# Kernel optimization log

Measured on AMD Instinct MI355X. Metric: run time of the kernel, lower is better.

## Reference

```python
import jax, jax.numpy as jnp
import numpy as np

B, H, W, C = 32, 56, 56, 192
WS, SS, NH = 7, 3, 6
HD = C // NH
SCALE = HD ** -0.5
N = WS * WS
NW = (H // WS) * (W // WS)
EPS = 1e-5


def _rel_pos_index():
    coords = np.stack(np.meshgrid(np.arange(WS), np.arange(WS), indexing='ij'))  # (2,WS,WS)
    cf = coords.reshape(2, -1)
    rel = cf[:, :, None] - cf[:, None, :]  # (2,N,N)
    rel = rel.transpose(1, 2, 0)
    rel[:, :, 0] += WS - 1
    rel[:, :, 1] += WS - 1
    rel[:, :, 0] *= 2 * WS - 1
    return rel.sum(-1)  # (N,N) int


def _attn_mask():
    img = np.zeros((H, W))
    cnt = 0
    for hs in (slice(0, -WS), slice(-WS, -SS), slice(-SS, None)):
        for ws in (slice(0, -WS), slice(-WS, -SS), slice(-SS, None)):
            img[hs, ws] = cnt
            cnt += 1
    win = img.reshape(H // WS, WS, W // WS, WS).transpose(0, 2, 1, 3).reshape(NW, N)
    diff = win[:, None, :] - win[:, :, None]
    return np.where(diff != 0, -100.0, 0.0).astype(np.float32)  # (NW,N,N)


REL_IDX = jnp.asarray(_rel_pos_index())
ATTN_MASK = jnp.asarray(_attn_mask())


def _ln(x, g, b):
    mu = x.mean(-1, keepdims=True)
    var = ((x - mu) ** 2).mean(-1, keepdims=True)
    return (x - mu) * jax.lax.rsqrt(var + EPS) * g + b


def setup_inputs() -> dict:
    key = jax.random.key(0)
    ks = jax.random.split(key, 8)
    d = {
        'x': jax.random.normal(ks[0], (B, H * W, C), jnp.float32),
        'norm1_g': jnp.ones((C,), jnp.float32),
        'norm1_b': jnp.zeros((C,), jnp.float32),
        'qkv_w': jax.random.normal(ks[1], (C, 3 * C), jnp.float32) * 0.02,
        'qkv_b': jnp.zeros((3 * C,), jnp.float32),
        'rpb_table': jax.random.normal(ks[2], ((2 * WS - 1) ** 2, NH), jnp.float32) * 0.02,
        'proj_w': jax.random.normal(ks[3], (C, C), jnp.float32) * 0.02,
        'proj_b': jnp.zeros((C,), jnp.float32),
        'norm2_g': jnp.ones((C,), jnp.float32),
        'norm2_b': jnp.zeros((C,), jnp.float32),
        'fc1_w': jax.random.normal(ks[4], (C, 4 * C), jnp.float32) * 0.02,
        'fc1_b': jnp.zeros((4 * C,), jnp.float32),
        'fc2_w': jax.random.normal(ks[5], (4 * C, C), jnp.float32) * 0.02,
        'fc2_b': jnp.zeros((C,), jnp.float32),
    }
    return d


def reference(x, norm1_g, norm1_b, qkv_w, qkv_b, rpb_table, proj_w, proj_b,
              norm2_g, norm2_b, fc1_w, fc1_b, fc2_w, fc2_b):
    shortcut = x
    h = _ln(x, norm1_g, norm1_b).reshape(B, H, W, C)
    # cyclic shift
    h = jnp.roll(h, (-SS, -SS), axis=(1, 2))
    # window partition -> (B*NW, N, C)
    hw = h.reshape(B, H // WS, WS, W // WS, WS, C).transpose(0, 1, 3, 2, 4, 5)
    hw = hw.reshape(B * NW, N, C)
    # qkv
    qkv = (hw @ qkv_w + qkv_b).reshape(B * NW, N, 3, NH, HD).transpose(2, 0, 3, 1, 4)
    q, k, v = qkv[0], qkv[1], qkv[2]  # (B_, NH, N, HD)
    attn = jnp.einsum('whnd,whmd->whnm', q * SCALE, k)
    bias = rpb_table[REL_IDX.reshape(-1)].reshape(N, N, NH).transpose(2, 0, 1)
    attn = attn + bias[None]
    # shift mask
    attn = attn.reshape(B, NW, NH, N, N) + ATTN_MASK[None, :, None]
    attn = jax.nn.softmax(attn.reshape(B * NW, NH, N, N), axis=-1)
    out = jnp.einsum('whnm,whmd->whnd', attn, v).transpose(0, 2, 1, 3).reshape(B * NW, N, C)
    out = out @ proj_w + proj_b
    # window reverse + unshift
    out = out.reshape(B, H // WS, W // WS, WS, WS, C).transpose(0, 1, 3, 2, 4, 5).reshape(B, H, W, C)
    out = jnp.roll(out, (SS, SS), axis=(1, 2)).reshape(B, H * W, C)
    x = shortcut + out
    # MLP
    m = _ln(x, norm2_g, norm2_b)
    m = jax.nn.gelu(m @ fc1_w + fc1_b, approximate=False) @ fc2_w + fc2_b
    return x + m
```

## Files before the change

### kernel.cpp

```cpp
#include <hip/hip_runtime.h>
#include <hip/hip_bf16.h>
#include <math.h>

#define MTOK 100352
#define SCALE_ 0.17677669529663687f

typedef short bf16x8 __attribute__((ext_vector_type(8)));
typedef float f32x4 __attribute__((ext_vector_type(4)));

__device__ __forceinline__ float b2f(unsigned short u) {
    return __uint_as_float(((unsigned int)u) << 16);
}
__device__ __forceinline__ unsigned short f2b(float f) {
    unsigned int u = __float_as_uint(f);
    unsigned int r = (u + 0x7FFFu + ((u >> 16) & 1u)) >> 16;
    return (unsigned short)r;
}
__device__ __forceinline__ void gload_lds16(const unsigned short* g, unsigned short* l) {
    __builtin_amdgcn_global_load_lds(
        (const __attribute__((address_space(1))) void*)g,
        (__attribute__((address_space(3))) void*)l, 16, 0, 0);
}

__global__ __launch_bounds__(256) void wconv_k(
    const float* __restrict__ w, unsigned short* __restrict__ wt, int K, int N)
{
    const int i = blockIdx.x * 256 + threadIdx.x;
    if (i >= N * K) return;
    const int n = i / K, k = i - n * K;
    wt[i] = f2b(w[(size_t)k * N + n]);
}

__global__ __launch_bounds__(256) void ln1_window_k(
    const float* __restrict__ x, const float* __restrict__ g,
    const float* __restrict__ bt, unsigned short* __restrict__ out)
{
    const int wid = (blockIdx.x * 256 + threadIdx.x) >> 6;
    if (wid >= MTOK) return;
    const int lane = threadIdx.x & 63;
    const int widx = wid / 49, n = wid - widx * 49;
    const int b = widx >> 6, win = widx & 63;
    const int wh = win >> 3, ww = win & 7;
    const int r = n / 7, cc = n - r * 7;
    int hh = wh * 7 + r + 3;  if (hh >= 56) hh -= 56;
    int wc = ww * 7 + cc + 3; if (wc >= 56) wc -= 56;
    const size_t src = ((size_t)b * 3136 + hh * 56 + wc) * 192;
    const float v0 = x[src + lane], v1 = x[src + lane + 64], v2 = x[src + lane + 128];
    float s1 = v0 + v1 + v2;
    float s2 = v0 * v0 + v1 * v1 + v2 * v2;
    #pragma unroll
    for (int off = 32; off; off >>= 1) {
        s1 += __shfl_xor(s1, off, 64);
        s2 += __shfl_xor(s2, off, 64);
    }
    const float mu = s1 * (1.f / 192.f);
    const float var = s2 * (1.f / 192.f) - mu * mu;
    const float rs = rsqrtf(var + 1e-5f);
    const size_t dst = (size_t)wid * 192;
    out[dst + lane]       = f2b((v0 - mu) * rs * g[lane]       + bt[lane]);
    out[dst + lane + 64]  = f2b((v1 - mu) * rs * g[lane + 64]  + bt[lane + 64]);
    out[dst + lane + 128] = f2b((v2 - mu) * rs * g[lane + 128] + bt[lane + 128]);
}

__global__ __launch_bounds__(256) void ln2_k(
    const float* __restrict__ x, const float* __restrict__ g,
    const float* __restrict__ bt, unsigned short* __restrict__ out)
{
    const int t = (blockIdx.x * 256 + threadIdx.x) >> 6;
    if (t >= MTOK) return;
    const int lane = threadIdx.x & 63;
    const size_t src = (size_t)t * 192;
    const float v0 = x[src + lane], v1 = x[src + lane + 64], v2 = x[src + lane + 128];
    float s1 = v0 + v1 + v2;
    float s2 = v0 * v0 + v1 * v1 + v2 * v2;
    #pragma unroll
    for (int off = 32; off; off >>= 1) {
        s1 += __shfl_xor(s1, off, 64);
        s2 += __shfl_xor(s2, off, 64);
    }
    const float mu = s1 * (1.f / 192.f);
    const float var = s2 * (1.f / 192.f) - mu * mu;
    const float rs = rsqrtf(var + 1e-5f);
    out[src + lane]       = f2b((v0 - mu) * rs * g[lane]       + bt[lane]);
    out[src + lane + 64]  = f2b((v1 - mu) * rs * g[lane + 64]  + bt[lane + 64]);
    out[src + lane + 128] = f2b((v2 - mu) * rs * g[lane + 128] + bt[lane + 128]);
}

enum { EPI_STORE_BF16 = 0, EPI_PROJ = 1, EPI_GELU = 2, EPI_RES = 3 };

template <int EPI>
__global__ __launch_bounds__(256) void mgemm_k(
    const unsigned short* __restrict__ A, const unsigned short* __restrict__ BT,
    const float* __restrict__ bias, unsigned short* __restrict__ outb,
    float* __restrict__ outf, const float* __restrict__ xres,
    int N, int K, int gx)
{
    __shared__ __align__(16) unsigned short As[2][128 * 32];
    __shared__ __align__(16) unsigned short Bs[2][64 * 32];

    const int nwg = gridDim.x;
    int lin = blockIdx.x;
    lin = (lin & 7) * (nwg >> 3) + (lin >> 3);
    const int bn = lin % gx, bm = lin / gx;
    const int row0 = bm * 128, col0 = bn * 64;

    const int tid = threadIdx.x;
    const int w = tid >> 6, lane = tid & 63;
    const int wr = w >> 1, wc = w & 1;
    const int l16 = lane & 15, l4 = lane >> 4;

    const unsigned short* Ab = A + (size_t)row0 * K;
    const unsigned short* Bb = BT + (size_t)col0 * K;
    const int sr = lane >> 2;
    const int sq = ((lane & 3) ^ ((lane >> 3) & 3)) * 8;

    #pragma unroll
    for (int i = 0; i < 2; i++) {
        const int ch = w * 2 + i;
        gload_lds16(Ab + (size_t)(ch * 16 + sr) * K + sq, &As[0][ch * 512 + lane * 8]);
    }
    gload_lds16(Bb + (size_t)(w * 16 + sr) * K + sq, &Bs[0][w * 512 + lane * 8]);
    __syncthreads();

    f32x4 acc[4][2];
    #pragma unroll
    for (int m = 0; m < 4; m++)
        #pragma unroll
        for (int n = 0; n < 2; n++) acc[m][n] = (f32x4){0.f, 0.f, 0.f, 0.f};

    const int rdc = (l4 ^ ((l16 >> 1) & 3)) * 8;
    const int nt = K >> 5;
    for (int t = 0; t < nt; ++t) {
        const int cur = t & 1;
        if (t + 1 < nt) {
            const int k0 = (t + 1) << 5;
            #pragma unroll
            for (int i = 0; i < 2; i++) {
                const int ch = w * 2 + i;
                gload_lds16(Ab + (size_t)(ch * 16 + sr) * K + k0 + sq,
                            &As[cur ^ 1][ch * 512 + lane * 8]);
            }
            gload_lds16(Bb + (size_t)(w * 16 + sr) * K + k0 + sq,
                        &Bs[cur ^ 1][w * 512 + lane * 8]);
        }
        bf16x8 af[4], bf[2];
        #pragma unroll
        for (int m = 0; m < 4; m++)
            af[m] = *reinterpret_cast<const bf16x8*>(
                &As[cur][(wr * 64 + m * 16 + l16) * 32 + rdc]);
        #pragma unroll
        for (int n = 0; n < 2; n++)
            bf[n] = *reinterpret_cast<const bf16x8*>(
                &Bs[cur][(wc * 32 + n * 16 + l16) * 32 + rdc]);
        #pragma unroll
        for (int m = 0; m < 4; m++)
            #pragma unroll
            for (int n = 0; n < 2; n++)
                acc[m][n] = __builtin_amdgcn_mfma_f32_16x16x32_bf16(
                    af[m], bf[n], acc[m][n], 0, 0, 0);
        __syncthreads();
    }

    float bv[2];
    #pragma unroll
    for (int n = 0; n < 2; n++) bv[n] = bias[col0 + wc * 32 + n * 16 + l16];

    #pragma unroll
    for (int m = 0; m < 4; m++) {
        #pragma unroll
        for (int j = 0; j < 4; j++) {
            const int row = row0 + wr * 64 + m * 16 + l4 * 4 + j;
            if constexpr (EPI == EPI_PROJ) {
                const int widx = row / 49, n49 = row - widx * 49;
                const int b = widx >> 6, win = widx & 63;
                const int wh = win >> 3, ww = win & 7;
                const int r = n49 / 7, cc = n49 - r * 7;
                int hh = wh * 7 + r + 3;  if (hh >= 56) hh -= 56;
                int wcc = ww * 7 + cc + 3; if (wcc >= 56) wcc -= 56;
                const size_t tok = ((size_t)b * 3136 + hh * 56 + wcc) * 192;
                #pragma unroll
                for (int n = 0; n < 2; n++) {
                    const int col = col0 + wc * 32 + n * 16 + l16;
                    outf[tok + col] = xres[tok + col] + acc[m][n][j] + bv[n];
                }
            } else if constexpr (EPI == EPI_STORE_BF16) {
                #pragma unroll
                for (int n = 0; n < 2; n++) {
                    const int col = col0 + wc * 32 + n * 16 + l16;
                    outb[(size_t)row * N + col] = f2b(acc[m][n][j] + bv[n]);
                }
            } else if constexpr (EPI == EPI_GELU) {
                #pragma unroll
                for (int n = 0; n < 2; n++) {
                    const int col = col0 + wc * 32 + n * 16 + l16;
                    float v = acc[m][n][j] + bv[n];
                    v = 0.5f * v * (1.f + erff(v * 0.70710678118654752f));
                    outb[(size_t)row * N + col] = f2b(v);
                }
            } else {
                #pragma unroll
                for (int n = 0; n < 2; n++) {
                    const int col = col0 + wc * 32 + n * 16 + l16;
                    outf[(size_t)row * N + col] += acc[m][n][j] + bv[n];
                }
            }
        }
    }
}

__global__ __launch_bounds__(64) void attn_mfma_k(
    const unsigned short* __restrict__ qkv, const float* __restrict__ rpb,
    unsigned short* __restrict__ out)
{
    const int blk = blockIdx.x;
    const int widx = blk / 6, head = blk - widx * 6;
    const int win = widx & 63;
    const int wh = win >> 3, ww = win & 7;

    __shared__ __align__(16) unsigned short vt[32 * 72];
    __shared__ __align__(16) unsigned short pl[64 * 72];
    __shared__ float bias_s[256];

    const int lane = threadIdx.x;
    const int l16 = lane & 15, l4 = lane >> 4;
    const size_t base = (size_t)widx * 49 * 576 + (size_t)head * 32;

    for (int i = lane; i < 169; i += 64) bias_s[i] = rpb[i * 6 + head];

    #pragma unroll
    for (int it = 0; it < 4; ++it) {
        const int c = lane + it * 64;
        const int m = c >> 2, d8 = (c & 3) * 8;
        bf16x8 v8 = {};
        if (m < 49)
            v8 = *reinterpret_cast<const bf16x8*>(qkv + base + (size_t)m * 576 + 384 + d8);
        #pragma unroll
        for (int r = 0; r < 8; ++r) vt[(d8 + r) * 72 + m] = (unsigned short)v8[r];
    }

    bf16x8 kf[4], qf[4];
    #pragma unroll
    for (int f = 0; f < 4; ++f) {
        const int rrow = f * 16 + l16;
        bf16x8 kz = {}, qz = {};
        if (rrow < 49) {
            kz = *reinterpret_cast<const bf16x8*>(qkv + base + (size_t)rrow * 576 + 192 + l4 * 8);
            qz = *reinterpret_cast<const bf16x8*>(qkv + base + (size_t)rrow * 576 + l4 * 8);
        }
        kf[f] = kz; qf[f] = qz;
    }

    f32x4 acc[4][4];
    #pragma unroll
    for (int mf = 0; mf < 4; ++mf)
        #pragma unroll
        for (int nf = 0; nf < 4; ++nf) {
            f32x4 z = (f32x4){0.f, 0.f, 0.f, 0.f};
            acc[mf][nf] = __builtin_amdgcn_mfma_f32_16x16x32_bf16(kf[mf], qf[nf], z, 0, 0, 0);
        }

    __syncthreads();

    int gn[4], labn[4]; bool nok[4];
    #pragma unroll
    for (int nf = 0; nf < 4; ++nf) {
        const int n = nf * 16 + l16;
        const int rn = (n * 9363) >> 16, cn = n - rn * 7;
        gn[nf] = n + 6 * rn;
        labn[nf] = (wh == 7 ? (rn < 4 ? 1 : 2) : 0) * 3 + (ww == 7 ? (cn < 4 ? 1 : 2) : 0);
        nok[nf] = (n < 49);
    }

    #pragma unroll
    for (int mf = 0; mf < 4; ++mf) {
        #pragma unroll
        for (int j = 0; j < 4; ++j) {
            const int m = mf * 16 + l4 * 4 + j;
            const int rm = (m * 9363) >> 16, cm = m - rm * 7;
            const int gm = m + 6 * rm;
            const int labm = (wh == 7 ? (rm < 4 ? 1 : 2) : 0) * 3 + (ww == 7 ? (cm < 4 ? 1 : 2) : 0);
            const bool mok = (m < 49);
            #pragma unroll
            for (int nf = 0; nf < 4; ++nf) {
                float s = -1e30f;
                if (mok && nok[nf]) {
                    s = acc[mf][nf][j] * SCALE_ + bias_s[gn[nf] - gm + 84];
                    if (labn[nf] != labm) s -= 100.f;
                }
                acc[mf][nf][j] = s;
            }
        }
    }

    #pragma unroll
    for (int nf = 0; nf < 4; ++nf) {
        float mx = -1e30f;
        #pragma unroll
        for (int mf = 0; mf < 4; ++mf)
            #pragma unroll
            for (int j = 0; j < 4; ++j) mx = fmaxf(mx, acc[mf][nf][j]);
        mx = fmaxf(mx, __shfl_xor(mx, 16, 64));
        mx = fmaxf(mx, __shfl_xor(mx, 32, 64));
        float sum = 0.f;
        #pragma unroll
        for (int mf = 0; mf < 4; ++mf)
            #pragma unroll
            for (int j = 0; j < 4; ++j) {
                const float e = __expf(acc[mf][nf][j] - mx);
                acc[mf][nf][j] = e;
                sum += e;
            }
        sum += __shfl_xor(sum, 16, 64);
        sum += __shfl_xor(sum, 32, 64);
        const float inv = 1.f / sum;
        const int n = nf * 16 + l16;
        #pragma unroll
        for (int mf = 0; mf < 4; ++mf)
            #pragma unroll
            for (int jp = 0; jp < 2; ++jp) {
                const int m = mf * 16 + l4 * 4 + jp * 2;
                const unsigned int pk =
                    (unsigned int)f2b(acc[mf][nf][jp * 2] * inv) |
                    ((unsigned int)f2b(acc[mf][nf][jp * 2 + 1] * inv) << 16);
                *reinterpret_cast<unsigned int*>(&pl[n * 72 + m]) = pk;
            }
    }
    __syncthreads();

    f32x4 oacc[4][2];
    #pragma unroll
    for (int nf = 0; nf < 4; ++nf)
        #pragma unroll
        for (int df = 0; df < 2; ++df) oacc[nf][df] = (f32x4){0.f, 0.f, 0.f, 0.f};
    #pragma unroll
    for (int ks = 0; ks < 2; ++ks) {
        bf16x8 vf[2];
        #pragma unroll
        for (int df = 0; df < 2; ++df)
            vf[df] = *reinterpret_cast<const bf16x8*>(&vt[(df * 16 + l16) * 72 + ks * 32 + l4 * 8]);
        #pragma unroll
        for (int nf = 0; nf < 4; ++nf) {
            const bf16x8 pf = *reinterpret_cast<const bf16x8*>(&pl[(nf * 16 + l16) * 72 + ks * 32 + l4 * 8]);
            #pragma unroll
            for (int df = 0; df < 2; ++df)
                oacc[nf][df] = __builtin_amdgcn_mfma_f32_16x16x32_bf16(pf, vf[df], oacc[nf][df], 0, 0, 0);
        }
    }

    #pragma unroll
    for (int nf = 0; nf < 4; ++nf)
        #pragma unroll
        for (int j = 0; j < 4; ++j) {
            const int n = nf * 16 + l4 * 4 + j;
            if (n < 49) {
                const size_t o = ((size_t)widx * 49 + n) * 192 + (size_t)head * 32;
                out[o + l16]      = f2b(oacc[nf][0][j]);
                out[o + 16 + l16] = f2b(oacc[nf][1][j]);
            }
        }
}

extern "C" void kernel_launch(void* const* d_in, const int* in_sizes, int n_in,
                              void* d_out, int out_size, void* d_ws, size_t ws_size,
                              hipStream_t stream)
{
    const float* x      = (const float*)d_in[0];
    const float* n1g    = (const float*)d_in[1];
    const float* n1b    = (const float*)d_in[2];
    const float* qkv_w  = (const float*)d_in[3];
    const float* qkv_b  = (const float*)d_in[4];
    const float* rpb    = (const float*)d_in[5];
    const float* proj_w = (const float*)d_in[6];
    const float* proj_b = (const float*)d_in[7];
    const float* n2g    = (const float*)d_in[8];
    const float* n2b    = (const float*)d_in[9];
    const float* fc1_w  = (const float*)d_in[10];
    const float* fc1_b  = (const float*)d_in[11];
    const float* fc2_w  = (const float*)d_in[12];
    const float* fc2_b  = (const float*)d_in[13];
    float* out = (float*)d_out;

    const int M = MTOK;
    unsigned short* big   = (unsigned short*)d_ws;
    unsigned short* winx  = big + (size_t)M * 768;
    unsigned short* qkvT  = winx + (size_t)M * 192;
    unsigned short* projT = qkvT + 576 * 192;
    unsigned short* fc1T  = projT + 192 * 192;
    unsigned short* fc2T  = fc1T + 768 * 192;

    wconv_k<<<(576 * 192 + 255) / 256, 256, 0, stream>>>(qkv_w, qkvT, 192, 576);
    wconv_k<<<(192 * 192 + 255) / 256, 256, 0, stream>>>(proj_w, projT, 192, 192);
    wconv_k<<<(768 * 192 + 255) / 256, 256, 0, stream>>>(fc1_w, fc1T, 192, 768);
    wconv_k<<<(192 * 768 + 255) / 256, 256, 0, stream>>>(fc2_w, fc2T, 768, 192);

    ln1_window_k<<<M / 4, 256, 0, stream>>>(x, n1g, n1b, winx);
    mgemm_k<EPI_STORE_BF16><<<9 * (M / 128), 256, 0, stream>>>(
        winx, qkvT, qkv_b, big, nullptr, nullptr, 576, 192, 9);
    attn_mfma_k<<<2048 * 6, 64, 0, stream>>>(big, rpb, winx);
    mgemm_k<EPI_PROJ><<<3 * (M / 128), 256, 0, stream>>>(
        winx, projT, proj_b, nullptr, out, x, 192, 192, 3);
    ln2_k<<<M / 4, 256, 0, stream>>>(out, n2g, n2b, winx);
    mgemm_k<EPI_GELU><<<12 * (M / 128), 256, 0, stream>>>(
        winx, fc1T, fc1_b, big, nullptr, nullptr, 768, 192, 12);
    mgemm_k<EPI_RES><<<3 * (M / 128), 256, 0, stream>>>(
        big, fc2T, fc2_b, nullptr, out, nullptr, 192, 768, 3);
}
```

Baseline: 374.8 us.

## Fuse projection GEMM with residual and LayerNorm2; use tanh GELU

Adds a projection kernel where each block computes all 192 output columns for 128 rows. Its epilogue adds the residual and bias, un-shifts the window layout, and applies LayerNorm2 using shuffles across the 16 column lanes. It writes both the fp32 residual stream and the bf16 normalized input for fc1, so the separate ln2 pass and its reread of the fp32 activations go away. The cost is a larger register and LDS footprint per block and a grid of only M/128 blocks. Separately, the exact erf GELU is replaced by a tanh-form approximation built on __expf, which is cheaper but numerically different from the reference's exact GELU.

```diff
diff --git a/kernel.cpp b/kernel.cpp
--- a/kernel.cpp
+++ b/kernel.cpp
@@ -62,38 +62,13 @@
     out[dst + lane + 128] = f2b((v2 - mu) * rs * g[lane + 128] + bt[lane + 128]);
 }
 
-__global__ __launch_bounds__(256) void ln2_k(
-    const float* __restrict__ x, const float* __restrict__ g,
-    const float* __restrict__ bt, unsigned short* __restrict__ out)
-{
-    const int t = (blockIdx.x * 256 + threadIdx.x) >> 6;
-    if (t >= MTOK) return;
-    const int lane = threadIdx.x & 63;
-    const size_t src = (size_t)t * 192;
-    const float v0 = x[src + lane], v1 = x[src + lane + 64], v2 = x[src + lane + 128];
-    float s1 = v0 + v1 + v2;
-    float s2 = v0 * v0 + v1 * v1 + v2 * v2;
-    #pragma unroll
-    for (int off = 32; off; off >>= 1) {
-        s1 += __shfl_xor(s1, off, 64);
-        s2 += __shfl_xor(s2, off, 64);
-    }
-    const float mu = s1 * (1.f / 192.f);
-    const float var = s2 * (1.f / 192.f) - mu * mu;
-    const float rs = rsqrtf(var + 1e-5f);
-    out[src + lane]       = f2b((v0 - mu) * rs * g[lane]       + bt[lane]);
-    out[src + lane + 64]  = f2b((v1 - mu) * rs * g[lane + 64]  + bt[lane + 64]);
-    out[src + lane + 128] = f2b((v2 - mu) * rs * g[lane + 128] + bt[lane + 128]);
-}
-
-enum { EPI_STORE_BF16 = 0, EPI_PROJ = 1, EPI_GELU = 2, EPI_RES = 3 };
+enum { EPI_STORE_BF16 = 0, EPI_GELU = 2, EPI_RES = 3 };
 
 template <int EPI>
 __global__ __launch_bounds__(256) void mgemm_k(
     const unsigned short* __restrict__ A, const unsigned short* __restrict__ BT,
     const float* __restrict__ bias, unsigned short* __restrict__ outb,
-    float* __restrict__ outf, const float* __restrict__ xres,
-    int N, int K, int gx)
+    float* __restrict__ outf, int N, int K, int gx)
 {
     __shared__ __align__(16) unsigned short As[2][128 * 32];
     __shared__ __align__(16) unsigned short Bs[2][64 * 32];
@@ -170,20 +145,7 @@
         #pragma unroll
         for (int j = 0; j < 4; j++) {
             const int row = row0 + wr * 64 + m * 16 + l4 * 4 + j;
-            if constexpr (EPI == EPI_PROJ) {
-                const int widx = row / 49, n49 = row - widx * 49;
-                const int b = widx >> 6, win = widx & 63;
-                const int wh = win >> 3, ww = win & 7;
-                const int r = n49 / 7, cc = n49 - r * 7;
-                int hh = wh * 7 + r + 3;  if (hh >= 56) hh -= 56;
-                int wcc = ww * 7 + cc + 3; if (wcc >= 56) wcc -= 56;
-                const size_t tok = ((size_t)b * 3136 + hh * 56 + wcc) * 192;
-                #pragma unroll
-                for (int n = 0; n < 2; n++) {
-                    const int col = col0 + wc * 32 + n * 16 + l16;
-                    outf[tok + col] = xres[tok + col] + acc[m][n][j] + bv[n];
-                }
-            } else if constexpr (EPI == EPI_STORE_BF16) {
+            if constexpr (EPI == EPI_STORE_BF16) {
                 #pragma unroll
                 for (int n = 0; n < 2; n++) {
                     const int col = col0 + wc * 32 + n * 16 + l16;
@@ -194,7 +156,9 @@
                 for (int n = 0; n < 2; n++) {
                     const int col = col0 + wc * 32 + n * 16 + l16;
                     float v = acc[m][n][j] + bv[n];
-                    v = 0.5f * v * (1.f + erff(v * 0.70710678118654752f));
+                    const float y = 0.7978845608028654f * (v + 0.044715f * v * v * v);
+                    const float e2 = __expf(2.f * y);
+                    v = 0.5f * v * (2.f - 2.f / (e2 + 1.f));
                     outb[(size_t)row * N + col] = f2b(v);
                 }
             } else {
@@ -203,6 +167,128 @@
                     const int col = col0 + wc * 32 + n * 16 + l16;
                     outf[(size_t)row * N + col] += acc[m][n][j] + bv[n];
                 }
+            }
+        }
+    }
+}
+
+__global__ __launch_bounds__(256) void projln_k(
+    const unsigned short* __restrict__ A, const unsigned short* __restrict__ BT,
+    const float* __restrict__ bias, const float* __restrict__ xres,
+    const float* __restrict__ g2, const float* __restrict__ b2,
+    float* __restrict__ x2, unsigned short* __restrict__ xn)
+{
+    constexpr int K = 192;
+    __shared__ __align__(16) unsigned short As[2][128 * 32];
+    __shared__ __align__(16) unsigned short Bs[2][192 * 32];
+
+    const int nwg = gridDim.x;
+    int lin = blockIdx.x;
+    lin = (lin & 7) * (nwg >> 3) + (lin >> 3);
+    const int row0 = lin * 128;
+
+    const int tid = threadIdx.x;
+    const int w = tid >> 6, lane = tid & 63;
+    const int l16 = lane & 15, l4 = lane >> 4;
+
+    const unsigned short* Ab = A + (size_t)row0 * K;
+    const int sr = lane >> 2;
+    const int sq = ((lane & 3) ^ ((lane >> 3) & 3)) * 8;
+
+    #pragma unroll
+    for (int i = 0; i < 2; i++) {
+        const int ch = w * 2 + i;
+        gload_lds16(Ab + (size_t)(ch * 16 + sr) * K + sq, &As[0][ch * 512 + lane * 8]);
+    }
+    #pragma unroll
+    for (int i = 0; i < 3; i++) {
+        const int ch = w * 3 + i;
+        gload_lds16(BT + (size_t)(ch * 16 + sr) * K + sq, &Bs[0][ch * 512 + lane * 8]);
+    }
+    __syncthreads();
+
+    f32x4 acc[2][12];
+    #pragma unroll
+    for (int m = 0; m < 2; m++)
+        #pragma unroll
+        for (int n = 0; n < 12; n++) acc[m][n] = (f32x4){0.f, 0.f, 0.f, 0.f};
+
+    const int rdc = (l4 ^ ((l16 >> 1) & 3)) * 8;
+    #pragma unroll
+    for (int t = 0; t < 6; ++t) {
+        const int cur = t & 1;
+        if (t + 1 < 6) {
+            const int k0 = (t + 1) << 5;
+            #pragma unroll
+            for (int i = 0; i < 2; i++) {
+                const int ch = w * 2 + i;
+                gload_lds16(Ab + (size_t)(ch * 16 + sr) * K + k0 + sq,
+                            &As[cur ^ 1][ch * 512 + lane * 8]);
+            }
+            #pragma unroll
+            for (int i = 0; i < 3; i++) {
+                const int ch = w * 3 + i;
+                gload_lds16(BT + (size_t)(ch * 16 + sr) * K + k0 + sq,
+                            &Bs[cur ^ 1][ch * 512 + lane * 8]);
+            }
+        }
+        bf16x8 af[2];
+        #pragma unroll
+        for (int m = 0; m < 2; m++)
+            af[m] = *reinterpret_cast<const bf16x8*>(
+                &As[cur][(w * 32 + m * 16 + l16) * 32 + rdc]);
+        #pragma unroll
+        for (int n = 0; n < 12; n++) {
+            const bf16x8 bf = *reinterpret_cast<const bf16x8*>(
+                &Bs[cur][(n * 16 + l16) * 32 + rdc]);
+            #pragma unroll
+            for (int m = 0; m < 2; m++)
+                acc[m][n] = __builtin_amdgcn_mfma_f32_16x16x32_bf16(
+                    af[m], bf, acc[m][n], 0, 0, 0);
+        }
+        __syncthreads();
+    }
+
+    float bv[12], gv[12], bb[12];
+    #pragma unroll
+    for (int n = 0; n < 12; n++) {
+        const int col = n * 16 + l16;
+        bv[n] = bias[col]; gv[n] = g2[col]; bb[n] = b2[col];
+    }
+
+    #pragma unroll
+    for (int m = 0; m < 2; m++) {
+        #pragma unroll
+        for (int j = 0; j < 4; j++) {
+            const int row = row0 + w * 32 + m * 16 + l4 * 4 + j;
+            const int widx = row / 49, n49 = row - widx * 49;
+            const int b = widx >> 6, win = widx & 63;
+            const int wh = win >> 3, ww = win & 7;
+            const int r = n49 / 7, cc = n49 - r * 7;
+            int hh = wh * 7 + r + 3;  if (hh >= 56) hh -= 56;
+            int wcc = ww * 7 + cc + 3; if (wcc >= 56) wcc -= 56;
+            const size_t tok = ((size_t)b * 3136 + hh * 56 + wcc) * 192;
+            float v[12];
+            float s1 = 0.f, s2 = 0.f;
+            #pragma unroll
+            for (int n = 0; n < 12; n++) {
+                v[n] = xres[tok + n * 16 + l16] + acc[m][n][j] + bv[n];
+                s1 += v[n];
+                s2 += v[n] * v[n];
+            }
+            #pragma unroll
+            for (int off = 1; off < 16; off <<= 1) {
+                s1 += __shfl_xor(s1, off, 64);
+                s2 += __shfl_xor(s2, off, 64);
+            }
+            const float mu = s1 * (1.f / 192.f);
+            const float var = s2 * (1.f / 192.f) - mu * mu;
+            const float rs = rsqrtf(var + 1e-5f);
+            #pragma unroll
+            for (int n = 0; n < 12; n++) {
+                const size_t o = tok + n * 16 + l16;
+                x2[o] = v[n];
+                xn[o] = f2b((v[n] - mu) * rs * gv[n] + bb[n]);
             }
         }
     }
@@ -387,6 +473,7 @@
     unsigned short* projT = qkvT + 576 * 192;
     unsigned short* fc1T  = projT + 192 * 192;
     unsigned short* fc2T  = fc1T + 768 * 192;
+    unsigned short* xn    = fc2T + 192 * 768;
 
     wconv_k<<<(576 * 192 + 255) / 256, 256, 0, stream>>>(qkv_w, qkvT, 192, 576);
     wconv_k<<<(192 * 192 + 255) / 256, 256, 0, stream>>>(proj_w, projT, 192, 192);
@@ -395,13 +482,12 @@
 
     ln1_window_k<<<M / 4, 256, 0, stream>>>(x, n1g, n1b, winx);
     mgemm_k<EPI_STORE_BF16><<<9 * (M / 128), 256, 0, stream>>>(
-        winx, qkvT, qkv_b, big, nullptr, nullptr, 576, 192, 9);
+        winx, qkvT, qkv_b, big, nullptr, 576, 192, 9);
     attn_mfma_k<<<2048 * 6, 64, 0, stream>>>(big, rpb, winx);
-    mgemm_k<EPI_PROJ><<<3 * (M / 128), 256, 0, stream>>>(
-        winx, projT, proj_b, nullptr, out, x, 192, 192, 3);
-    ln2_k<<<M / 4, 256, 0, stream>>>(out, n2g, n2b, winx);
+    projln_k<<<M / 128, 256, 0, stream>>>(
+        winx, projT, proj_b, x, n2g, n2b, out, xn);
     mgemm_k<EPI_GELU><<<12 * (M / 128), 256, 0, stream>>>(
-        winx, fc1T, fc1_b, big, nullptr, nullptr, 768, 192, 12);
+        xn, fc1T, fc1_b, big, nullptr, 768, 192, 12);
     mgemm_k<EPI_RES><<<3 * (M / 128), 256, 0, stream>>>(
-        big, fc2T, fc2_b, nullptr, out, nullptr, 192, 768, 3);
-}
+        big, fc2T, fc2_b, nullptr, out, 192, 768, 3);
+}
```

New measurement: 405.5 us. +8.2%, slower.

## Load full K=192 tile into LDS per GEMM block and use tanh-form GELU

Applied to the files above, without the earlier changes.

The GEMM kernel now takes K as a template parameter. Instead of a double-buffered 32-wide K loop with a barrier per step, it loads 192-wide K chunks of A and B into shared memory at once, so the K=192 GEMMs need a single load and barrier. The exact erf GELU is replaced with the tanh approximation, computed through a fast exp and reciprocal. Shared memory per block grows to about 72KB, which may lower occupancy and removes the overlap between loads and MMA. The GELU approximation also changes numerics slightly.

```diff
diff --git a/kernel.cpp b/kernel.cpp
--- a/kernel.cpp
+++ b/kernel.cpp
@@ -88,15 +88,16 @@
 
 enum { EPI_STORE_BF16 = 0, EPI_PROJ = 1, EPI_GELU = 2, EPI_RES = 3 };
 
-template <int EPI>
+template <int EPI, int K>
 __global__ __launch_bounds__(256) void mgemm_k(
     const unsigned short* __restrict__ A, const unsigned short* __restrict__ BT,
     const float* __restrict__ bias, unsigned short* __restrict__ outb,
     float* __restrict__ outf, const float* __restrict__ xres,
-    int N, int K, int gx)
-{
-    __shared__ __align__(16) unsigned short As[2][128 * 32];
-    __shared__ __align__(16) unsigned short Bs[2][64 * 32];
+    int N, int gx)
+{
+    constexpr int NKC = K / 192;
+    __shared__ __align__(16) unsigned short As[128 * 192];
+    __shared__ __align__(16) unsigned short Bs[64 * 192];
 
     const int nwg = gridDim.x;
     int lin = blockIdx.x;
@@ -113,14 +114,7 @@
     const unsigned short* Bb = BT + (size_t)col0 * K;
     const int sr = lane >> 2;
     const int sq = ((lane & 3) ^ ((lane >> 3) & 3)) * 8;
-
-    #pragma unroll
-    for (int i = 0; i < 2; i++) {
-        const int ch = w * 2 + i;
-        gload_lds16(Ab + (size_t)(ch * 16 + sr) * K + sq, &As[0][ch * 512 + lane * 8]);
-    }
-    gload_lds16(Bb + (size_t)(w * 16 + sr) * K + sq, &Bs[0][w * 512 + lane * 8]);
-    __syncthreads();
+    const int rdc = (l4 ^ ((l16 >> 1) & 3)) * 8;
 
     f32x4 acc[4][2];
     #pragma unroll
@@ -128,37 +122,42 @@
         #pragma unroll
         for (int n = 0; n < 2; n++) acc[m][n] = (f32x4){0.f, 0.f, 0.f, 0.f};
 
-    const int rdc = (l4 ^ ((l16 >> 1) & 3)) * 8;
-    const int nt = K >> 5;
-    for (int t = 0; t < nt; ++t) {
-        const int cur = t & 1;
-        if (t + 1 < nt) {
-            const int k0 = (t + 1) << 5;
-            #pragma unroll
-            for (int i = 0; i < 2; i++) {
-                const int ch = w * 2 + i;
-                gload_lds16(Ab + (size_t)(ch * 16 + sr) * K + k0 + sq,
-                            &As[cur ^ 1][ch * 512 + lane * 8]);
-            }
-            gload_lds16(Bb + (size_t)(w * 16 + sr) * K + k0 + sq,
-                        &Bs[cur ^ 1][w * 512 + lane * 8]);
-        }
-        bf16x8 af[4], bf[2];
-        #pragma unroll
-        for (int m = 0; m < 4; m++)
-            af[m] = *reinterpret_cast<const bf16x8*>(
-                &As[cur][(wr * 64 + m * 16 + l16) * 32 + rdc]);
-        #pragma unroll
-        for (int n = 0; n < 2; n++)
-            bf[n] = *reinterpret_cast<const bf16x8*>(
-                &Bs[cur][(wc * 32 + n * 16 + l16) * 32 + rdc]);
-        #pragma unroll
-        for (int m = 0; m < 4; m++)
+    for (int kc = 0; kc < NKC; ++kc) {
+        const int kbase = kc * 192;
+        if (kc) __syncthreads();
+        #pragma unroll
+        for (int i = 0; i < 12; i++) {
+            const int idx = w * 12 + i;
+            const int ks = idx >> 3, ch = idx & 7;
+            gload_lds16(Ab + (size_t)(ch * 16 + sr) * K + kbase + ks * 32 + sq,
+                        &As[ks * 4096 + ch * 512 + lane * 8]);
+        }
+        #pragma unroll
+        for (int i = 0; i < 6; i++) {
+            const int idx = w * 6 + i;
+            const int ks = idx >> 2, rg = idx & 3;
+            gload_lds16(Bb + (size_t)(rg * 16 + sr) * K + kbase + ks * 32 + sq,
+                        &Bs[ks * 2048 + rg * 512 + lane * 8]);
+        }
+        __syncthreads();
+        #pragma unroll
+        for (int ks = 0; ks < 6; ++ks) {
+            bf16x8 af[4], bf[2];
+            #pragma unroll
+            for (int m = 0; m < 4; m++)
+                af[m] = *reinterpret_cast<const bf16x8*>(
+                    &As[ks * 4096 + (wr * 64 + m * 16 + l16) * 32 + rdc]);
             #pragma unroll
             for (int n = 0; n < 2; n++)
-                acc[m][n] = __builtin_amdgcn_mfma_f32_16x16x32_bf16(
-                    af[m], bf[n], acc[m][n], 0, 0, 0);
-        __syncthreads();
+                bf[n] = *reinterpret_cast<const bf16x8*>(
+                    &Bs[ks * 2048 + (wc * 32 + n * 16 + l16) * 32 + rdc]);
+            #pragma unroll
+            for (int m = 0; m < 4; m++)
+                #pragma unroll
+                for (int n = 0; n < 2; n++)
+                    acc[m][n] = __builtin_amdgcn_mfma_f32_16x16x32_bf16(
+                        af[m], bf[n], acc[m][n], 0, 0, 0);
+        }
     }
 
     float bv[2];
@@ -194,7 +193,10 @@
                 for (int n = 0; n < 2; n++) {
                     const int col = col0 + wc * 32 + n * 16 + l16;
                     float v = acc[m][n][j] + bv[n];
-                    v = 0.5f * v * (1.f + erff(v * 0.70710678118654752f));
+                    const float wv = v + 0.044715f * v * v * v;
+                    const float sg = __builtin_amdgcn_rcpf(
+                        1.f + __expf(-1.5957691216057308f * wv));
+                    v = v * sg;
                     outb[(size_t)row * N + col] = f2b(v);
                 }
             } else {
@@ -394,14 +396,14 @@
     wconv_k<<<(192 * 768 + 255) / 256, 256, 0, stream>>>(fc2_w, fc2T, 768, 192);
 
     ln1_window_k<<<M / 4, 256, 0, stream>>>(x, n1g, n1b, winx);
-    mgemm_k<EPI_STORE_BF16><<<9 * (M / 128), 256, 0, stream>>>(
-        winx, qkvT, qkv_b, big, nullptr, nullptr, 576, 192, 9);
+    mgemm_k<EPI_STORE_BF16, 192><<<9 * (M / 128), 256, 0, stream>>>(
+        winx, qkvT, qkv_b, big, nullptr, nullptr, 576, 9);
     attn_mfma_k<<<2048 * 6, 64, 0, stream>>>(big, rpb, winx);
-    mgemm_k<EPI_PROJ><<<3 * (M / 128), 256, 0, stream>>>(
-        winx, projT, proj_b, nullptr, out, x, 192, 192, 3);
+    mgemm_k<EPI_PROJ, 192><<<3 * (M / 128), 256, 0, stream>>>(
+        winx, projT, proj_b, nullptr, out, x, 192, 3);
     ln2_k<<<M / 4, 256, 0, stream>>>(out, n2g, n2b, winx);
-    mgemm_k<EPI_GELU><<<12 * (M / 128), 256, 0, stream>>>(
-        winx, fc1T, fc1_b, big, nullptr, nullptr, 768, 192, 12);
-    mgemm_k<EPI_RES><<<3 * (M / 128), 256, 0, stream>>>(
-        big, fc2T, fc2_b, nullptr, out, nullptr, 192, 768, 3);
-}
+    mgemm_k<EPI_GELU, 192><<<12 * (M / 128), 256, 0, stream>>>(
+        winx, fc1T, fc1_b, big, nullptr, nullptr, 768, 12);
+    mgemm_k<EPI_RES, 768><<<3 * (M / 128), 256, 0, stream>>>(
+        big, fc2T, fc2_b, nullptr, out, nullptr, 192, 3);
+}
```

Result: slower. 399.3 us (+6.5%).
